# Optimization experiments

Measured on AMD Instinct MI355X. Metric: run time of the kernel, lower is better.

Reference implementation:

```python
import jax, jax.numpy as jnp
import numpy as np

N_NODES = 20000
N_EDGES = 320000
N_GRAPHS = 128


def gat_conv(x, W, attn_l, attn_r, bias, src, dst, num_nodes):
    """DGL-style GATConv: per-edge attention, edge softmax over incoming
    edges of each destination node, scatter-sum aggregation."""
    H, D = attn_l.shape
    feat = (x @ W).reshape(-1, H, D)                      # [N,H,D]
    el = jnp.sum(feat * attn_l, axis=-1)                  # [N,H]
    er = jnp.sum(feat * attn_r, axis=-1)                  # [N,H]
    e = jax.nn.leaky_relu(el[src] + er[dst], 0.2)         # [E,H]
    # numerically stable segment softmax over dst
    m = jax.ops.segment_max(e, dst, num_segments=num_nodes)   # [N,H]
    e_exp = jnp.exp(e - m[dst])                               # [E,H]
    denom = jax.ops.segment_sum(e_exp, dst, num_segments=num_nodes)
    alpha = e_exp / denom[dst]                                 # [E,H]
    msg = alpha[:, :, None] * feat[src]                        # [E,H,D]
    rst = jax.ops.segment_sum(msg, dst, num_segments=num_nodes)  # [N,H,D]
    return rst + bias.reshape(1, H, D)


def setup_inputs() -> dict:
    key = jax.random.key(0)
    ks = jax.random.split(key, 12)
    s1 = 1.0 / np.sqrt(256.0)
    s2 = 1.0 / np.sqrt(512.0)
    return {
        "x": jax.random.normal(ks[0], (N_NODES, 256), dtype=jnp.float32),
        "W1": jax.random.normal(ks[1], (256, 512), dtype=jnp.float32) * s1,
        "a_l1": jax.random.normal(ks[2], (8, 64), dtype=jnp.float32) * 0.1,
        "a_r1": jax.random.normal(ks[3], (8, 64), dtype=jnp.float32) * 0.1,
        "b1": jnp.zeros((512,), dtype=jnp.float32),
        "W2": jax.random.normal(ks[4], (512, 128), dtype=jnp.float32) * s2,
        "a_l2": jax.random.normal(ks[5], (1, 128), dtype=jnp.float32) * 0.1,
        "a_r2": jax.random.normal(ks[6], (1, 128), dtype=jnp.float32) * 0.1,
        "b2": jnp.zeros((128,), dtype=jnp.float32),
        "edge_src": jax.random.randint(ks[7], (N_EDGES,), 0, N_NODES, dtype=jnp.int32),
        "edge_dst": jax.random.randint(ks[8], (N_EDGES,), 0, N_NODES, dtype=jnp.int32),
        "graph_ids": jnp.sort(jax.random.randint(ks[9], (N_NODES,), 0, N_GRAPHS, dtype=jnp.int32)),
    }


def reference(x, W1, a_l1, a_r1, b1, W2, a_l2, a_r2, b2, edge_src, edge_dst, graph_ids):
    h = gat_conv(x, W1, a_l1, a_r1, b1, edge_src, edge_dst, N_NODES)  # [N,8,64]
    h = h.reshape(N_NODES, -1)                                        # flatten(1)
    h = gat_conv(h, W2, a_l2, a_r2, b2, edge_src, edge_dst, N_NODES)  # [N,1,128]
    # dgl.mean_nodes: per-graph mean pooling
    ones = jnp.ones((N_NODES,), dtype=h.dtype)
    counts = jax.ops.segment_sum(ones, graph_ids, num_segments=N_GRAPHS)
    sums = jax.ops.segment_sum(h, graph_ids, num_segments=N_GRAPHS)   # [G,1,128]
    hg = sums / jnp.maximum(counts, 1.0)[:, None, None]
    return hg
```

## Files before the change

### kernel.cpp

```cpp
#include <hip/hip_runtime.h>
#include <hip/hip_fp16.h>

#define N_NODES  20000
#define N_EDGES  320000
#define N_GRAPHS 128

typedef _Float16 half8 __attribute__((ext_vector_type(8)));
typedef float    f32x4 __attribute__((ext_vector_type(4)));

__global__ void fill_zero(float* __restrict__ p, int n) {
    int i = blockIdx.x * blockDim.x + threadIdx.x;
    int stride = gridDim.x * blockDim.x;
    for (; i < n; i += stride) p[i] = 0.f;
}

__global__ void transpose_both(const float* __restrict__ W1, const float* __restrict__ W2,
                               __half* __restrict__ w1t, __half* __restrict__ w2t) {
    int i = blockIdx.x * blockDim.x + threadIdx.x;
    if (i < 256 * 512) {
        int r = i >> 9, c = i & 511;
        w1t[c * 256 + r] = __float2half(W1[i]);
    } else {
        int j = i - 256 * 512;
        if (j < 512 * 128) {
            int r = j >> 7, c = j & 127;
            w2t[c * 512 + r] = __float2half(W2[j]);
        }
    }
}

template <int BM, int BN, int WM, int WN, int H, int D, bool AF32>
__global__ __launch_bounds__(256) void gemm_mfma(
        const void* __restrict__ A_, const __half* __restrict__ BT,
        __half* __restrict__ C, const float* __restrict__ al,
        const float* __restrict__ ar, float* __restrict__ el,
        float* __restrict__ er, int Mm, int Nn, int Kk) {
    constexpr int BK  = 32;
    constexpr int MFR = WM / 16, NFR = WN / 16;
    constexpr int WCOLS = BN / WN;
    __shared__ __align__(16) __half As[BM * BK];
    __shared__ __align__(16) __half Bs[BN * BK];
    const int tid  = threadIdx.x;
    const int w    = tid >> 6, lane = tid & 63;
    const int wr   = w / WCOLS, wc = w % WCOLS;
    const int brow = blockIdx.x * BM;
    const int bcol = blockIdx.y * BN;
    const int lr   = lane & 15;
    const int lk   = (lane >> 4) * 8;

    f32x4 acc[MFR][NFR] = {};

    for (int k0 = 0; k0 < Kk; k0 += BK) {
        for (int c = tid; c < BM * 4; c += 256) {
            int r = c >> 2, ko = (c & 3) * 8;
            int gr = brow + r; if (gr >= Mm) gr = Mm - 1;
            int off = (r * BK + ko) ^ ((r & 7) << 3);
            if constexpr (AF32) {
                const float* ap = (const float*)A_ + (size_t)gr * Kk + k0 + ko;
                float4 v0 = *reinterpret_cast<const float4*>(ap);
                float4 v1 = *reinterpret_cast<const float4*>(ap + 4);
                union { __half2 h2[4]; uint4 u; } pk;
                pk.h2[0] = __floats2half2_rn(v0.x, v0.y);
                pk.h2[1] = __floats2half2_rn(v0.z, v0.w);
                pk.h2[2] = __floats2half2_rn(v1.x, v1.y);
                pk.h2[3] = __floats2half2_rn(v1.z, v1.w);
                *reinterpret_cast<uint4*>(&As[off]) = pk.u;
            } else {
                *reinterpret_cast<uint4*>(&As[off]) =
                    *reinterpret_cast<const uint4*>((const __half*)A_ + (size_t)gr * Kk + k0 + ko);
            }
        }
        for (int c = tid; c < BN * 4; c += 256) {
            int r = c >> 2, ko = (c & 3) * 8;
            int off = (r * BK + ko) ^ ((r & 7) << 3);
            *reinterpret_cast<uint4*>(&Bs[off]) =
                *reinterpret_cast<const uint4*>(&BT[(size_t)(bcol + r) * Kk + k0 + ko]);
        }
        __syncthreads();
        half8 af[MFR], bf[NFR];
#pragma unroll
        for (int m = 0; m < MFR; ++m) {
            int r = wr * WM + m * 16 + lr;
            af[m] = *reinterpret_cast<const half8*>(&As[(r * BK + lk) ^ ((r & 7) << 3)]);
        }
#pragma unroll
        for (int n = 0; n < NFR; ++n) {
            int r = wc * WN + n * 16 + lr;
            bf[n] = *reinterpret_cast<const half8*>(&Bs[(r * BK + lk) ^ ((r & 7) << 3)]);
        }
#pragma unroll
        for (int m = 0; m < MFR; ++m)
#pragma unroll
            for (int n = 0; n < NFR; ++n)
                acc[m][n] = __builtin_amdgcn_mfma_f32_16x16x32_f16(af[m], bf[n], acc[m][n], 0, 0, 0);
        __syncthreads();
    }

#pragma unroll
    for (int m = 0; m < MFR; ++m) {
        int r0 = brow + wr * WM + m * 16 + ((lane >> 4) << 2);
#pragma unroll
        for (int n = 0; n < NFR; ++n) {
            int cc = bcol + wc * WN + n * 16 + lr;
#pragma unroll
            for (int g = 0; g < 4; ++g)
                if (r0 + g < Mm) C[(size_t)(r0 + g) * Nn + cc] = __float2half(acc[m][n][g]);
        }
    }
    const int h = (bcol + wc * WN) / D;
    float alv[NFR], arv[NFR];
#pragma unroll
    for (int n = 0; n < NFR; ++n) {
        alv[n] = al[bcol + wc * WN + n * 16 + lr];
        arv[n] = ar[bcol + wc * WN + n * 16 + lr];
    }
#pragma unroll
    for (int m = 0; m < MFR; ++m) {
#pragma unroll
        for (int g = 0; g < 4; ++g) {
            float pl = 0.f, pr = 0.f;
#pragma unroll
            for (int n = 0; n < NFR; ++n) {
                pl += acc[m][n][g] * alv[n];
                pr += acc[m][n][g] * arv[n];
            }
            pl += __shfl_xor(pl, 1); pl += __shfl_xor(pl, 2);
            pl += __shfl_xor(pl, 4); pl += __shfl_xor(pl, 8);
            pr += __shfl_xor(pr, 1); pr += __shfl_xor(pr, 2);
            pr += __shfl_xor(pr, 4); pr += __shfl_xor(pr, 8);
            int gr = brow + wr * WM + m * 16 + ((lane >> 4) << 2) + g;
            if (lr == 0 && gr < Mm) {
                if constexpr (WN == D) {
                    el[(size_t)gr * H + h] = pl;
                    er[(size_t)gr * H + h] = pr;
                } else {
                    atomicAdd(&el[(size_t)gr * H + h], pl);
                    atomicAdd(&er[(size_t)gr * H + h], pr);
                }
            }
        }
    }
}

__global__ void hist_kernel(const int* __restrict__ dst, int* __restrict__ deg, int E) {
    int e = blockIdx.x * blockDim.x + threadIdx.x;
    if (e >= E) return;
    atomicAdd(&deg[dst[e]], 1);
}

__global__ void scan_kernel(const int* __restrict__ deg, int* __restrict__ rowptr, int n) {
    __shared__ int partial[1024];
    const int t = threadIdx.x;
    const int CH = (n + 1023) / 1024;
    const int base = t * CH;
    int local = 0;
    for (int i = 0; i < CH; ++i)
        if (base + i < n) local += deg[base + i];
    partial[t] = local;
    __syncthreads();
    for (int o = 1; o < 1024; o <<= 1) {
        int v = (t >= o) ? partial[t - o] : 0;
        __syncthreads();
        partial[t] += v;
        __syncthreads();
    }
    int run = (t == 0) ? 0 : partial[t - 1];
    for (int i = 0; i < CH; ++i) {
        if (base + i <= n) rowptr[base + i] = run;
        if (base + i < n) run += deg[base + i];
    }
}

__global__ void scatter_kernel(const int* __restrict__ src, const int* __restrict__ dst,
                               const int* __restrict__ rowptr, int* __restrict__ cursor,
                               int* __restrict__ esrc, int* __restrict__ edst, int E) {
    int e = blockIdx.x * blockDim.x + threadIdx.x;
    if (e >= E) return;
    int d = dst[e];
    int pos = rowptr[d] + atomicAdd(&cursor[d], 1);
    esrc[pos] = src[e];
    edst[pos] = d;
}

__global__ void edge_w8(const float* __restrict__ el, const float* __restrict__ er,
                        const int* __restrict__ esrc, const int* __restrict__ edst,
                        float* __restrict__ w, int E) {
    int p = blockIdx.x * blockDim.x + threadIdx.x;
    if (p >= E) return;
    int s = esrc[p], d = edst[p];
    float4 l0 = *reinterpret_cast<const float4*>(&el[s * 8]);
    float4 l1 = *reinterpret_cast<const float4*>(&el[s * 8 + 4]);
    float4 r0 = *reinterpret_cast<const float4*>(&er[d * 8]);
    float4 r1 = *reinterpret_cast<const float4*>(&er[d * 8 + 4]);
    float xs[8] = {l0.x + r0.x, l0.y + r0.y, l0.z + r0.z, l0.w + r0.w,
                   l1.x + r1.x, l1.y + r1.y, l1.z + r1.z, l1.w + r1.w};
    float o[8];
#pragma unroll
    for (int h = 0; h < 8; ++h) {
        float x = xs[h];
        x = (x > 0.f) ? x : 0.2f * x;
        o[h] = __expf(x);
    }
    *reinterpret_cast<float4*>(&w[(size_t)p * 8])     = make_float4(o[0], o[1], o[2], o[3]);
    *reinterpret_cast<float4*>(&w[(size_t)p * 8 + 4]) = make_float4(o[4], o[5], o[6], o[7]);
}

__global__ void edge_w1(const float* __restrict__ el, const float* __restrict__ er,
                        const int* __restrict__ esrc, const int* __restrict__ edst,
                        float* __restrict__ w, int E) {
    int p = blockIdx.x * blockDim.x + threadIdx.x;
    if (p >= E) return;
    float x = el[esrc[p]] + er[edst[p]];
    x = (x > 0.f) ? x : 0.2f * x;
    w[p] = __expf(x);
}

template <int F, int H, bool HOUT>
__global__ __launch_bounds__(256) void node_aggr_wave(
        const __half* __restrict__ feat, const float* __restrict__ wbuf,
        const int* __restrict__ rowptr, const int* __restrict__ esrc,
        const float* __restrict__ bias, void* __restrict__ rst_, int N) {
    constexpr int LPN = F / 8;
    constexpr int NPW = 64 / LPN;
    constexpr int D   = F / H;
    const int wid  = (blockIdx.x * blockDim.x + threadIdx.x) >> 6;
    const int lane = threadIdx.x & 63;
    const int n    = wid * NPW + lane / LPN;
    if (n >= N) return;
    const int col = (lane % LPN) * 8;
    const int h   = col / D;
    const int rs = rowptr[n], re = rowptr[n + 1];
    const __half* fq = feat + col;

    float acc[8] = {};
    float dsum = 0.f;
    int i = rs;
    for (; i + 4 <= re; i += 4) {
        int s0 = esrc[i], s1 = esrc[i + 1], s2 = esrc[i + 2], s3 = esrc[i + 3];
        float w0 = (H > 1) ? wbuf[(size_t)i * H + h]       : wbuf[i];
        float w1 = (H > 1) ? wbuf[(size_t)(i + 1) * H + h] : wbuf[i + 1];
        float w2 = (H > 1) ? wbuf[(size_t)(i + 2) * H + h] : wbuf[i + 2];
        float w3 = (H > 1) ? wbuf[(size_t)(i + 3) * H + h] : wbuf[i + 3];
        union { uint4 u; __half2 h2[4]; } r0, r1, r2, r3;
        r0.u = *reinterpret_cast<const uint4*>(fq + (size_t)s0 * F);
        r1.u = *reinterpret_cast<const uint4*>(fq + (size_t)s1 * F);
        r2.u = *reinterpret_cast<const uint4*>(fq + (size_t)s2 * F);
        r3.u = *reinterpret_cast<const uint4*>(fq + (size_t)s3 * F);
        dsum += (w0 + w1) + (w2 + w3);
#pragma unroll
        for (int k = 0; k < 4; ++k) {
            float2 f0 = __half22float2(r0.h2[k]);
            float2 f1 = __half22float2(r1.h2[k]);
            float2 f2 = __half22float2(r2.h2[k]);
            float2 f3 = __half22float2(r3.h2[k]);
            acc[2 * k]     += w0 * f0.x + w1 * f1.x + w2 * f2.x + w3 * f3.x;
            acc[2 * k + 1] += w0 * f0.y + w1 * f1.y + w2 * f2.y + w3 * f3.y;
        }
    }
    for (; i < re; ++i) {
        int s = esrc[i];
        float w = (H > 1) ? wbuf[(size_t)i * H + h] : wbuf[i];
        union { uint4 u; __half2 h2[4]; } r;
        r.u = *reinterpret_cast<const uint4*>(fq + (size_t)s * F);
        dsum += w;
#pragma unroll
        for (int k = 0; k < 4; ++k) {
            float2 f = __half22float2(r.h2[k]);
            acc[2 * k]     += w * f.x;
            acc[2 * k + 1] += w * f.y;
        }
    }
    float inv = (re > rs) ? 1.f / dsum : 0.f;
    float4 b0 = *reinterpret_cast<const float4*>(bias + col);
    float4 b1 = *reinterpret_cast<const float4*>(bias + col + 4);
    float o[8] = {acc[0] * inv + b0.x, acc[1] * inv + b0.y,
                  acc[2] * inv + b0.z, acc[3] * inv + b0.w,
                  acc[4] * inv + b1.x, acc[5] * inv + b1.y,
                  acc[6] * inv + b1.z, acc[7] * inv + b1.w};
    if constexpr (HOUT) {
        union { __half2 h2[4]; uint4 u; } pk;
        pk.h2[0] = __floats2half2_rn(o[0], o[1]);
        pk.h2[1] = __floats2half2_rn(o[2], o[3]);
        pk.h2[2] = __floats2half2_rn(o[4], o[5]);
        pk.h2[3] = __floats2half2_rn(o[6], o[7]);
        *reinterpret_cast<uint4*>((__half*)rst_ + (size_t)n * F + col) = pk.u;
    } else {
        float* op = (float*)rst_ + (size_t)n * F + col;
        *reinterpret_cast<float4*>(op)     = make_float4(o[0], o[1], o[2], o[3]);
        *reinterpret_cast<float4*>(op + 4) = make_float4(o[4], o[5], o[6], o[7]);
    }
}

__global__ void graph_start_kernel(const int* __restrict__ gid, int* __restrict__ start,
                                   int N, int G) {
    int g = blockIdx.x * blockDim.x + threadIdx.x;
    if (g > G) return;
    if (g == G) { start[G] = N; return; }
    int lo = 0, hi = N;
    while (lo < hi) {
        int mid = (lo + hi) >> 1;
        if (gid[mid] < g) lo = mid + 1; else hi = mid;
    }
    start[g] = lo;
}

__global__ __launch_bounds__(1024) void seg_pool_kernel(
        const float* __restrict__ h, const int* __restrict__ start,
        float* __restrict__ out, int D) {
    __shared__ float part[7][128];
    int g = blockIdx.x;
    int d = threadIdx.x & 127;
    int j = threadIdx.x >> 7;
    int s = start[g], e = start[g + 1];
    float acc = 0.f;
    for (int n = s + j; n < e; n += 8) acc += h[(size_t)n * D + d];
    if (j > 0) part[j - 1][d] = acc;
    __syncthreads();
    if (j == 0) {
#pragma unroll
        for (int k = 0; k < 7; ++k) acc += part[k][d];
        out[(size_t)g * D + d] = acc / fmaxf((float)(e - s), 1.f);
    }
}

extern "C" void kernel_launch(void* const* d_in, const int* in_sizes, int n_in,
                              void* d_out, int out_size, void* d_ws, size_t ws_size,
                              hipStream_t stream) {
    const float* x   = (const float*)d_in[0];
    const float* W1  = (const float*)d_in[1];
    const float* al1 = (const float*)d_in[2];
    const float* ar1 = (const float*)d_in[3];
    const float* b1  = (const float*)d_in[4];
    const float* W2  = (const float*)d_in[5];
    const float* al2 = (const float*)d_in[6];
    const float* ar2 = (const float*)d_in[7];
    const float* b2  = (const float*)d_in[8];
    const int* src   = (const int*)d_in[9];
    const int* dst   = (const int*)d_in[10];
    const int* gid   = (const int*)d_in[11];
    float* out = (float*)d_out;

    float* ws = (float*)d_ws;
    size_t off = 0;
    int*   deg    = (int*)(ws + off); off += N_NODES;
    int*   cursor = (int*)(ws + off); off += N_NODES;
    float* el2    = ws + off;         off += N_NODES;
    float* er2    = ws + off;         off += N_NODES;
    const size_t zeroN = off;
    int* rowptr = (int*)(ws + off); off += N_NODES + 4;
    int* gstart = (int*)(ws + off); off += N_GRAPHS + 4;
    int* esrc   = (int*)(ws + off); off += N_EDGES;
    int* edst   = (int*)(ws + off); off += N_EDGES;
    float* w1buf = ws + off; off += (size_t)8 * N_EDGES;
    float* w2buf = ws + off; off += N_EDGES;
    __half* w1t    = (__half*)(ws + off); off += 512 * 256 / 2;
    __half* w2t    = (__half*)(ws + off); off += 128 * 512 / 2;
    __half* feat1h = (__half*)(ws + off); off += (size_t)N_NODES * 256;
    float*  el1    = ws + off; off += (size_t)N_NODES * 8;
    float*  er1    = ws + off; off += (size_t)N_NODES * 8;
    __half* rst1h  = (__half*)(ws + off); off += (size_t)N_NODES * 256;
    __half* feat2h = (__half*)(ws + off); off += (size_t)N_NODES * 64;
    float*  rst2   = ws + off; off += (size_t)N_NODES * 128;

    fill_zero<<<208, 256, 0, stream>>>(ws, (int)zeroN);

    hist_kernel<<<(N_EDGES + 255) / 256, 256, 0, stream>>>(dst, deg, N_EDGES);
    scan_kernel<<<1, 1024, 0, stream>>>(deg, rowptr, N_NODES);
    scatter_kernel<<<(N_EDGES + 255) / 256, 256, 0, stream>>>(src, dst, rowptr, cursor, esrc, edst, N_EDGES);
    graph_start_kernel<<<1, 256, 0, stream>>>(gid, gstart, N_NODES, N_GRAPHS);
    transpose_both<<<(256 * 512 + 512 * 128 + 255) / 256, 256, 0, stream>>>(W1, W2, w1t, w2t);

    dim3 g1((N_NODES + 127) / 128, 512 / 128);
    gemm_mfma<128, 128, 64, 64, 8, 64, true><<<g1, 256, 0, stream>>>(
        x, w1t, feat1h, al1, ar1, el1, er1, N_NODES, 512, 256);
    edge_w8<<<(N_EDGES + 255) / 256, 256, 0, stream>>>(el1, er1, esrc, edst, w1buf, N_EDGES);
    node_aggr_wave<512, 8, true><<<(N_NODES * 64 + 255) / 256, 256, 0, stream>>>(
        feat1h, w1buf, rowptr, esrc, b1, rst1h, N_NODES);

    dim3 g2((N_NODES + 63) / 64, 128 / 128);
    gemm_mfma<64, 128, 32, 64, 1, 128, false><<<g2, 256, 0, stream>>>(
        rst1h, w2t, feat2h, al2, ar2, el2, er2, N_NODES, 128, 512);
    edge_w1<<<(N_EDGES + 255) / 256, 256, 0, stream>>>(el2, er2, esrc, edst, w2buf, N_EDGES);
    node_aggr_wave<128, 1, false><<<(N_NODES * 16 + 255) / 256, 256, 0, stream>>>(
        feat2h, w2buf, rowptr, esrc, b2, rst2, N_NODES);

    seg_pool_kernel<<<N_GRAPHS, 1024, 0, stream>>>(rst2, gstart, out, 128);
}
```

Measured before the change: 208.9 us.

## Fuse edge attention weights into aggregation and merge setup kernels

Removes the separate edge_w8/edge_w1 kernels and their per-edge weight buffers. The node aggregation kernels now gather el[src], add the node's er, then apply leaky-relu and exp inline. This drops the destination-sorted edst array, one kernel launch per layer and the write/read of the per-edge weight buffers, at the cost of recomputing the exp in every lane that shares a head. It also folds the graph-start search into the weight-transpose setup kernel, shrinks the zero-fill to exclude el2/er2, and retiles the second GEMM so one warp covers all 128 output columns.

```diff
diff --git a/kernel.cpp b/kernel.cpp
--- a/kernel.cpp
+++ b/kernel.cpp
@@ -8,23 +8,33 @@
 typedef _Float16 half8 __attribute__((ext_vector_type(8)));
 typedef float    f32x4 __attribute__((ext_vector_type(4)));
 
-__global__ void fill_zero(float* __restrict__ p, int n) {
+__global__ void fill_zero(int* __restrict__ p, int n) {
     int i = blockIdx.x * blockDim.x + threadIdx.x;
     int stride = gridDim.x * blockDim.x;
-    for (; i < n; i += stride) p[i] = 0.f;
-}
-
-__global__ void transpose_both(const float* __restrict__ W1, const float* __restrict__ W2,
-                               __half* __restrict__ w1t, __half* __restrict__ w2t) {
+    for (; i < n; i += stride) p[i] = 0;
+}
+
+__global__ void setup_misc(const float* __restrict__ W1, const float* __restrict__ W2,
+                           __half* __restrict__ w1t, __half* __restrict__ w2t,
+                           const int* __restrict__ gid, int* __restrict__ gstart) {
     int i = blockIdx.x * blockDim.x + threadIdx.x;
     if (i < 256 * 512) {
         int r = i >> 9, c = i & 511;
         w1t[c * 256 + r] = __float2half(W1[i]);
+    } else if (i < 256 * 512 + 512 * 128) {
+        int j = i - 256 * 512;
+        int r = j >> 7, c = j & 127;
+        w2t[c * 512 + r] = __float2half(W2[j]);
     } else {
-        int j = i - 256 * 512;
-        if (j < 512 * 128) {
-            int r = j >> 7, c = j & 127;
-            w2t[c * 512 + r] = __float2half(W2[j]);
+        int g = i - (256 * 512 + 512 * 128);
+        if (g <= N_GRAPHS) {
+            if (g == N_GRAPHS) { gstart[N_GRAPHS] = N_NODES; return; }
+            int lo = 0, hi = N_NODES;
+            while (lo < hi) {
+                int mid = (lo + hi) >> 1;
+                if (gid[mid] < g) lo = mid + 1; else hi = mid;
+            }
+            gstart[g] = lo;
         }
     }
 }
@@ -173,53 +183,20 @@
 
 __global__ void scatter_kernel(const int* __restrict__ src, const int* __restrict__ dst,
                                const int* __restrict__ rowptr, int* __restrict__ cursor,
-                               int* __restrict__ esrc, int* __restrict__ edst, int E) {
+                               int* __restrict__ esrc, int E) {
     int e = blockIdx.x * blockDim.x + threadIdx.x;
     if (e >= E) return;
     int d = dst[e];
     int pos = rowptr[d] + atomicAdd(&cursor[d], 1);
     esrc[pos] = src[e];
-    edst[pos] = d;
-}
-
-__global__ void edge_w8(const float* __restrict__ el, const float* __restrict__ er,
-                        const int* __restrict__ esrc, const int* __restrict__ edst,
-                        float* __restrict__ w, int E) {
-    int p = blockIdx.x * blockDim.x + threadIdx.x;
-    if (p >= E) return;
-    int s = esrc[p], d = edst[p];
-    float4 l0 = *reinterpret_cast<const float4*>(&el[s * 8]);
-    float4 l1 = *reinterpret_cast<const float4*>(&el[s * 8 + 4]);
-    float4 r0 = *reinterpret_cast<const float4*>(&er[d * 8]);
-    float4 r1 = *reinterpret_cast<const float4*>(&er[d * 8 + 4]);
-    float xs[8] = {l0.x + r0.x, l0.y + r0.y, l0.z + r0.z, l0.w + r0.w,
-                   l1.x + r1.x, l1.y + r1.y, l1.z + r1.z, l1.w + r1.w};
-    float o[8];
-#pragma unroll
-    for (int h = 0; h < 8; ++h) {
-        float x = xs[h];
-        x = (x > 0.f) ? x : 0.2f * x;
-        o[h] = __expf(x);
-    }
-    *reinterpret_cast<float4*>(&w[(size_t)p * 8])     = make_float4(o[0], o[1], o[2], o[3]);
-    *reinterpret_cast<float4*>(&w[(size_t)p * 8 + 4]) = make_float4(o[4], o[5], o[6], o[7]);
-}
-
-__global__ void edge_w1(const float* __restrict__ el, const float* __restrict__ er,
-                        const int* __restrict__ esrc, const int* __restrict__ edst,
-                        float* __restrict__ w, int E) {
-    int p = blockIdx.x * blockDim.x + threadIdx.x;
-    if (p >= E) return;
-    float x = el[esrc[p]] + er[edst[p]];
-    x = (x > 0.f) ? x : 0.2f * x;
-    w[p] = __expf(x);
 }
 
 template <int F, int H, bool HOUT>
 __global__ __launch_bounds__(256) void node_aggr_wave(
-        const __half* __restrict__ feat, const float* __restrict__ wbuf,
-        const int* __restrict__ rowptr, const int* __restrict__ esrc,
-        const float* __restrict__ bias, void* __restrict__ rst_, int N) {
+        const __half* __restrict__ feat, const float* __restrict__ el,
+        const float* __restrict__ er, const int* __restrict__ rowptr,
+        const int* __restrict__ esrc, const float* __restrict__ bias,
+        void* __restrict__ rst_, int N) {
     constexpr int LPN = F / 8;
     constexpr int NPW = 64 / LPN;
     constexpr int D   = F / H;
@@ -229,6 +206,7 @@
     if (n >= N) return;
     const int col = (lane % LPN) * 8;
     const int h   = col / D;
+    const float ern = er[(size_t)n * H + h];
     const int rs = rowptr[n], re = rowptr[n + 1];
     const __half* fq = feat + col;
 
@@ -237,10 +215,15 @@
     int i = rs;
     for (; i + 4 <= re; i += 4) {
         int s0 = esrc[i], s1 = esrc[i + 1], s2 = esrc[i + 2], s3 = esrc[i + 3];
-        float w0 = (H > 1) ? wbuf[(size_t)i * H + h]       : wbuf[i];
-        float w1 = (H > 1) ? wbuf[(size_t)(i + 1) * H + h] : wbuf[i + 1];
-        float w2 = (H > 1) ? wbuf[(size_t)(i + 2) * H + h] : wbuf[i + 2];
-        float w3 = (H > 1) ? wbuf[(size_t)(i + 3) * H + h] : wbuf[i + 3];
+        float x0 = el[(size_t)s0 * H + h] + ern;
+        float x1 = el[(size_t)s1 * H + h] + ern;
+        float x2 = el[(size_t)s2 * H + h] + ern;
+        float x3 = el[(size_t)s3 * H + h] + ern;
+        x0 = (x0 > 0.f) ? x0 : 0.2f * x0;
+        x1 = (x1 > 0.f) ? x1 : 0.2f * x1;
+        x2 = (x2 > 0.f) ? x2 : 0.2f * x2;
+        x3 = (x3 > 0.f) ? x3 : 0.2f * x3;
+        float w0 = __expf(x0), w1 = __expf(x1), w2 = __expf(x2), w3 = __expf(x3);
         union { uint4 u; __half2 h2[4]; } r0, r1, r2, r3;
         r0.u = *reinterpret_cast<const uint4*>(fq + (size_t)s0 * F);
         r1.u = *reinterpret_cast<const uint4*>(fq + (size_t)s1 * F);
@@ -259,7 +242,9 @@
     }
     for (; i < re; ++i) {
         int s = esrc[i];
-        float w = (H > 1) ? wbuf[(size_t)i * H + h] : wbuf[i];
+        float x = el[(size_t)s * H + h] + ern;
+        x = (x > 0.f) ? x : 0.2f * x;
+        float w = __expf(x);
         union { uint4 u; __half2 h2[4]; } r;
         r.u = *reinterpret_cast<const uint4*>(fq + (size_t)s * F);
         dsum += w;
@@ -291,19 +276,6 @@
     }
 }
 
-__global__ void graph_start_kernel(const int* __restrict__ gid, int* __restrict__ start,
-                                   int N, int G) {
-    int g = blockIdx.x * blockDim.x + threadIdx.x;
-    if (g > G) return;
-    if (g == G) { start[G] = N; return; }
-    int lo = 0, hi = N;
-    while (lo < hi) {
-        int mid = (lo + hi) >> 1;
-        if (gid[mid] < g) lo = mid + 1; else hi = mid;
-    }
-    start[g] = lo;
-}
-
 __global__ __launch_bounds__(1024) void seg_pool_kernel(
         const float* __restrict__ h, const int* __restrict__ start,
         float* __restrict__ out, int D) {
@@ -342,17 +314,12 @@
 
     float* ws = (float*)d_ws;
     size_t off = 0;
-    int*   deg    = (int*)(ws + off); off += N_NODES;
-    int*   cursor = (int*)(ws + off); off += N_NODES;
-    float* el2    = ws + off;         off += N_NODES;
-    float* er2    = ws + off;         off += N_NODES;
+    int* deg    = (int*)(ws + off); off += N_NODES;
+    int* cursor = (int*)(ws + off); off += N_NODES;
     const size_t zeroN = off;
     int* rowptr = (int*)(ws + off); off += N_NODES + 4;
     int* gstart = (int*)(ws + off); off += N_GRAPHS + 4;
     int* esrc   = (int*)(ws + off); off += N_EDGES;
-    int* edst   = (int*)(ws + off); off += N_EDGES;
-    float* w1buf = ws + off; off += (size_t)8 * N_EDGES;
-    float* w2buf = ws + off; off += N_EDGES;
     __half* w1t    = (__half*)(ws + off); off += 512 * 256 / 2;
     __half* w2t    = (__half*)(ws + off); off += 128 * 512 / 2;
     __half* feat1h = (__half*)(ws + off); off += (size_t)N_NODES * 256;
@@ -360,29 +327,29 @@
     float*  er1    = ws + off; off += (size_t)N_NODES * 8;
     __half* rst1h  = (__half*)(ws + off); off += (size_t)N_NODES * 256;
     __half* feat2h = (__half*)(ws + off); off += (size_t)N_NODES * 64;
+    float*  el2    = ws + off; off += N_NODES;
+    float*  er2    = ws + off; off += N_NODES;
     float*  rst2   = ws + off; off += (size_t)N_NODES * 128;
 
-    fill_zero<<<208, 256, 0, stream>>>(ws, (int)zeroN);
+    fill_zero<<<40, 256, 0, stream>>>((int*)ws, (int)zeroN);
 
     hist_kernel<<<(N_EDGES + 255) / 256, 256, 0, stream>>>(dst, deg, N_EDGES);
     scan_kernel<<<1, 1024, 0, stream>>>(deg, rowptr, N_NODES);
-    scatter_kernel<<<(N_EDGES + 255) / 256, 256, 0, stream>>>(src, dst, rowptr, cursor, esrc, edst, N_EDGES);
-    graph_start_kernel<<<1, 256, 0, stream>>>(gid, gstart, N_NODES, N_GRAPHS);
-    transpose_both<<<(256 * 512 + 512 * 128 + 255) / 256, 256, 0, stream>>>(W1, W2, w1t, w2t);
+    scatter_kernel<<<(N_EDGES + 255) / 256, 256, 0, stream>>>(src, dst, rowptr, cursor, esrc, N_EDGES);
+    setup_misc<<<(256 * 512 + 512 * 128 + N_GRAPHS + 1 + 255) / 256, 256, 0, stream>>>(
+        W1, W2, w1t, w2t, gid, gstart);
 
     dim3 g1((N_NODES + 127) / 128, 512 / 128);
     gemm_mfma<128, 128, 64, 64, 8, 64, true><<<g1, 256, 0, stream>>>(
         x, w1t, feat1h, al1, ar1, el1, er1, N_NODES, 512, 256);
-    edge_w8<<<(N_EDGES + 255) / 256, 256, 0, stream>>>(el1, er1, esrc, edst, w1buf, N_EDGES);
     node_aggr_wave<512, 8, true><<<(N_NODES * 64 + 255) / 256, 256, 0, stream>>>(
-        feat1h, w1buf, rowptr, esrc, b1, rst1h, N_NODES);
+        feat1h, el1, er1, rowptr, esrc, b1, rst1h, N_NODES);
 
     dim3 g2((N_NODES + 63) / 64, 128 / 128);
-    gemm_mfma<64, 128, 32, 64, 1, 128, false><<<g2, 256, 0, stream>>>(
+    gemm_mfma<64, 128, 16, 128, 1, 128, false><<<g2, 256, 0, stream>>>(
         rst1h, w2t, feat2h, al2, ar2, el2, er2, N_NODES, 128, 512);
-    edge_w1<<<(N_EDGES + 255) / 256, 256, 0, stream>>>(el2, er2, esrc, edst, w2buf, N_EDGES);
     node_aggr_wave<128, 1, false><<<(N_NODES * 16 + 255) / 256, 256, 0, stream>>>(
-        feat2h, w2buf, rowptr, esrc, b2, rst2, N_NODES);
+        feat2h, el2, er2, rowptr, esrc, b2, rst2, N_NODES);
 
     seg_pool_kernel<<<N_GRAPHS, 1024, 0, stream>>>(rst2, gstart, out, 128);
 }
```

Measured after the change: 198.0 us. -5.2%, faster.
